# Kernel optimization log

Hardware: AMD Instinct MI355X
Metric: run time of the kernel (lower is better)

Reference implementation:

```python
import jax, jax.numpy as jnp
import numpy as np

D_MODEL = 1024
NUM_HEADS = 16
D_HEAD = D_MODEL // NUM_HEADS
D_FF = 4096
BATCH = 2
SEQ = 2048
EPS = 1e-5


def setup_inputs() -> dict:
    key = jax.random.key(0)
    ks = jax.random.split(key, 10)
    def tn(k, shape, std):
        # truncated normal in [-3*std, 3*std]
        return std * jax.random.truncated_normal(k, -3.0, 3.0, shape, dtype=jnp.float32)
    sd_attn = float(np.sqrt(2.0 / (D_MODEL + D_MODEL)))
    sd_ff1 = float(np.sqrt(2.0 / (D_MODEL + D_FF)))
    sd_ff2 = float(np.sqrt(2.0 / (D_FF + D_MODEL)))
    return {
        "x": jax.random.normal(ks[0], (BATCH, SEQ, D_MODEL), dtype=jnp.float32),
        "Wq": tn(ks[1], (D_MODEL, D_MODEL), sd_attn),
        "Wk": tn(ks[2], (D_MODEL, D_MODEL), sd_attn),
        "Wv": tn(ks[3], (D_MODEL, D_MODEL), sd_attn),
        "Wo": tn(ks[4], (D_MODEL, D_MODEL), sd_attn),
        "W1": tn(ks[5], (D_FF, D_MODEL), sd_ff1),
        "W2": tn(ks[6], (D_MODEL, D_FF), sd_ff2),
        "W3": tn(ks[7], (D_FF, D_MODEL), sd_ff1),
        "g1": tn(ks[8], (D_MODEL,), 1.0),
        "g2": tn(ks[9], (D_MODEL,), 1.0),
    }


def rmsnorm(x, g):
    xf = x.astype(jnp.float32)
    rms = jnp.sqrt(jnp.mean(xf * xf, axis=-1, keepdims=True) + EPS)
    return (xf / rms * g).astype(x.dtype)


def attention(x, Wq, Wk, Wv, Wo):
    B, S, D = x.shape
    def heads(t):  # [B,S,D] -> [B,H,S,dh]
        return t.reshape(B, S, NUM_HEADS, D_HEAD).transpose(0, 2, 1, 3)
    q = heads(jnp.einsum('oi,bsi->bso', Wq, x))
    k = heads(jnp.einsum('oi,bsi->bso', Wk, x))
    v = heads(jnp.einsum('oi,bsi->bso', Wv, x))
    logits = jnp.einsum('bhqd,bhkd->bhqk', q, k)
    mask = jnp.tril(jnp.ones((S, S), dtype=bool))
    logits = jnp.where(mask, logits, -jnp.inf)
    attn = jax.nn.softmax(logits / jnp.sqrt(jnp.float32(D_HEAD)), axis=-1)
    o = jnp.einsum('bhqk,bhkd->bhqd', attn, v)
    o = o.transpose(0, 2, 1, 3).reshape(B, S, D)
    return jnp.einsum('oi,bsi->bso', Wo, o)


def swiglu(x, W1, W2, W3):
    h1 = jnp.einsum('fi,bsi->bsf', W1, x)
    h3 = jnp.einsum('fi,bsi->bsf', W3, x)
    h = h1 * jax.nn.sigmoid(h1) * h3
    return jnp.einsum('of,bsf->bso', W2, h)


def reference(x, Wq, Wk, Wv, Wo, W1, W2, W3, g1, g2):
    x = x + attention(rmsnorm(x, g1), Wq, Wk, Wv, Wo)
    x = x + swiglu(rmsnorm(x, g2), W1, W2, W3)
    return x
```

## Files before the change

kernel.cpp:

```cpp
#include <hip/hip_runtime.h>
#include <hip/hip_bf16.h>

#define DM 1024
#define NH 16
#define DH 64
#define DFF 4096
#define NBATCH 2
#define SEQL 2048
#define MTOK (NBATCH*SEQL)

typedef float f32x4 __attribute__((ext_vector_type(4)));
typedef __bf16 bf16x8 __attribute__((ext_vector_type(8)));
typedef unsigned short u16;
typedef unsigned int u32;
typedef unsigned short u16x4 __attribute__((ext_vector_type(4)));
typedef unsigned short u16x8 __attribute__((ext_vector_type(8)));
typedef unsigned int u32x4 __attribute__((ext_vector_type(4)));

__device__ __forceinline__ u16 f2bf(float f) {
    u32 u = __builtin_bit_cast(u32, f);
    return (u16)((u + 0x7fffu + ((u >> 16) & 1u)) >> 16);
}
__device__ __forceinline__ float bf2f(u16 h) {
    return __builtin_bit_cast(float, (u32)h << 16);
}
__device__ __forceinline__ f32x4 mfma16(bf16x8 a, bf16x8 b, f32x4 c) {
    return __builtin_amdgcn_mfma_f32_16x16x32_bf16(a, b, c, 0, 0, 0);
}
__device__ __forceinline__ void gload16(const void* g, void* l) {
    __builtin_amdgcn_global_load_lds(
        (const __attribute__((address_space(1))) unsigned int*)g,
        (__attribute__((address_space(3))) unsigned int*)l, 16, 0, 0);
}
__device__ __forceinline__ int xcd_swz(int p, int nwg) {
    return (p & 7) * (nwg >> 3) + (p >> 3);
}
#define WAIT_VM8_BAR  { asm volatile("s_waitcnt vmcnt(8)" ::: "memory"); \
                        asm volatile("s_barrier" ::: "memory"); }
#define WAIT_VM0_BAR  { asm volatile("s_waitcnt vmcnt(0)" ::: "memory"); \
                        asm volatile("s_barrier" ::: "memory"); }
#define LGKM0_BAR     { asm volatile("s_waitcnt lgkmcnt(0)" ::: "memory"); \
                        asm volatile("s_barrier" ::: "memory"); }

__device__ __forceinline__ void gemm_core(
    const u16* __restrict__ Ah, const u16* __restrict__ Al,
    const u16* __restrict__ Bh, const u16* __restrict__ Bl,
    int K, int m0, int n0,
    u16* lsAh, u16* lsAl, u16* lsBh, u16* lsBl,
    f32x4 acc[4][4])
{
    const int t = threadIdx.x;
    const int lane = t & 63;
    const int wv = t >> 6;
    const int wm = ((t >> 7) & 1) * 64;
    const int wn = ((t >> 6) & 1) * 64;
    const int lrow = lane & 15;
    const int lk = lane >> 4;
    const f32x4 FZ = {0.f, 0.f, 0.f, 0.f};
#pragma unroll
    for (int i = 0; i < 4; ++i)
#pragma unroll
        for (int j = 0; j < 4; ++j) acc[i][j] = FZ;

    const int NT = K >> 5;
    const int rsub = lane >> 2;
    const int gchk = ((lane & 3) ^ ((lane >> 3) & 3)) * 8;
    const int rsw = (lk ^ ((lrow >> 1) & 3)) * 8;

    auto stage = [&](int buf, int kt) {
        const int k0 = kt << 5;
#pragma unroll
        for (int p = 0; p < 2; ++p) {
            const int seg = wv * 2 + p;
            const int row = seg * 16 + rsub;
            const size_t sa = (size_t)(m0 + row) * K + k0 + gchk;
            const size_t sb = (size_t)(n0 + row) * K + k0 + gchk;
            const int d = buf * 4096 + seg * 512;
            gload16(Ah + sa, lsAh + d);
            gload16(Al + sa, lsAl + d);
            gload16(Bh + sb, lsBh + d);
            gload16(Bl + sb, lsBl + d);
        }
    };

    stage(0, 0);
    int buf = 0;
    for (int kt = 0; kt < NT; ++kt) {
        if (kt + 1 < NT) {
            stage(buf ^ 1, kt + 1);
            WAIT_VM8_BAR
        } else {
            WAIT_VM0_BAR
        }
        bf16x8 ah[4], al[4], bh[4], bl[4];
#pragma unroll
        for (int i = 0; i < 4; ++i) {
            const int ia = buf * 4096 + (wm + i * 16 + lrow) * 32 + rsw;
            ah[i] = *reinterpret_cast<const bf16x8*>(&lsAh[ia]);
            al[i] = *reinterpret_cast<const bf16x8*>(&lsAl[ia]);
            const int ib = buf * 4096 + (wn + i * 16 + lrow) * 32 + rsw;
            bh[i] = *reinterpret_cast<const bf16x8*>(&lsBh[ib]);
            bl[i] = *reinterpret_cast<const bf16x8*>(&lsBl[ib]);
        }
        __builtin_amdgcn_s_setprio(1);
#pragma unroll
        for (int i = 0; i < 4; ++i)
#pragma unroll
            for (int j = 0; j < 4; ++j) {
                acc[i][j] = mfma16(ah[i], bh[j], acc[i][j]);
                acc[i][j] = mfma16(al[i], bh[j], acc[i][j]);
                acc[i][j] = mfma16(ah[i], bl[j], acc[i][j]);
            }
        __builtin_amdgcn_s_setprio(0);
        LGKM0_BAR
        buf ^= 1;
    }
}

#define GEMM_LDS \
    __shared__ __align__(16) u16 lsAh[2 * 4096], lsAl[2 * 4096], \
                                 lsBh[2 * 4096], lsBl[2 * 4096];

template <class F>
__device__ __forceinline__ void epilogue(const f32x4 acc[4][4], int m0, int n0, F f) {
    const int lane = threadIdx.x & 63;
    const int wm = ((threadIdx.x >> 7) & 1) * 64;
    const int wn = ((threadIdx.x >> 6) & 1) * 64;
#pragma unroll
    for (int i = 0; i < 4; ++i)
#pragma unroll
        for (int j = 0; j < 4; ++j)
#pragma unroll
            for (int r = 0; r < 4; ++r) {
                const int m = m0 + wm + i * 16 + ((lane >> 4) << 2) + r;
                const int o = n0 + wn + j * 16 + (lane & 15);
                f(m, o, acc[i][j][r]);
            }
}

struct WJobs { const float* s[7]; u16* h[7]; u16* l[7]; };
__global__ __launch_bounds__(256) void k_splitw_all(WJobs jobs)
{
    const int bid = blockIdx.x;
    int which, off;
    if (bid < 2048) { which = bid >> 9; off = bid & 511; }
    else { which = 4 + ((bid - 2048) >> 11); off = (bid - 2048) & 2047; }
    const float* __restrict__ src = jobs.s[which];
    u16* __restrict__ dh = jobs.h[which];
    u16* __restrict__ dl = jobs.l[which];
    const int i = (off * 256 + threadIdx.x) * 8;
    const f32x4 a = *reinterpret_cast<const f32x4*>(src + i);
    const f32x4 b = *reinterpret_cast<const f32x4*>(src + i + 4);
    u16x8 hh, ll;
#pragma unroll
    for (int e = 0; e < 4; ++e) {
        const u16 h0 = f2bf(a[e]);
        hh[e] = h0; ll[e] = f2bf(a[e] - bf2f(h0));
        const u16 h1 = f2bf(b[e]);
        hh[4 + e] = h1; ll[4 + e] = f2bf(b[e] - bf2f(h1));
    }
    *reinterpret_cast<u16x8*>(dh + i) = hh;
    *reinterpret_cast<u16x8*>(dl + i) = ll;
}

__global__ __launch_bounds__(256) void k_rmsnorm(
    const float* __restrict__ x, const float* __restrict__ g,
    u16* __restrict__ oh, u16* __restrict__ ol)
{
    const int row = blockIdx.x * 4 + (threadIdx.x >> 6);
    const int lane = threadIdx.x & 63;
    const float* xr = x + (size_t)row * DM;
    f32x4 v[4];
    float ss = 0.f;
#pragma unroll
    for (int j = 0; j < 4; ++j) {
        v[j] = *reinterpret_cast<const f32x4*>(&xr[(lane + j * 64) * 4]);
        ss += v[j][0] * v[j][0] + v[j][1] * v[j][1] + v[j][2] * v[j][2] + v[j][3] * v[j][3];
    }
#pragma unroll
    for (int off = 32; off > 0; off >>= 1) ss += __shfl_xor(ss, off, 64);
    const float sc = 1.0f / sqrtf(ss * (1.0f / (float)DM) + 1e-5f);
#pragma unroll
    for (int j = 0; j < 4; ++j) {
        const int c0 = (lane + j * 64) * 4;
        const f32x4 gv = *reinterpret_cast<const f32x4*>(&g[c0]);
        u16x4 hh, ll;
#pragma unroll
        for (int e = 0; e < 4; ++e) {
            const float y = v[j][e] * sc * gv[e];
            const u16 hi = f2bf(y);
            hh[e] = hi;
            ll[e] = f2bf(y - bf2f(hi));
        }
        *reinterpret_cast<u16x4*>(&oh[(size_t)row * DM + c0]) = hh;
        *reinterpret_cast<u16x4*>(&ol[(size_t)row * DM + c0]) = ll;
    }
}

__global__ __launch_bounds__(256, 2) void k_qkv(
    const u16* __restrict__ Ah, const u16* __restrict__ Al,
    const u16* __restrict__ swqh, const u16* __restrict__ swql,
    const u16* __restrict__ swkh, const u16* __restrict__ swkl,
    const u16* __restrict__ swvh, const u16* __restrict__ swvl,
    u16* __restrict__ qh, u16* __restrict__ ql, u16* __restrict__ kh, u16* __restrict__ kl,
    u16* __restrict__ vth, u16* __restrict__ vtl)
{
    GEMM_LDS
    const int swz = xcd_swz(blockIdx.y * 32 + blockIdx.x, 32 * 24);
    const int m0 = (swz & 31) * 128;
    const int ng = (swz >> 5) * 128;
    const int proj = ng >> 10;
    const int n0 = ng & 1023;
    const u16* Bh = (proj == 0) ? swqh : ((proj == 1) ? swkh : swvh);
    const u16* Bl = (proj == 0) ? swql : ((proj == 1) ? swkl : swvl);
    f32x4 acc[4][4];
    gemm_core(Ah, Al, Bh, Bl, DM, m0, n0, lsAh, lsAl, lsBh, lsBl, acc);
    if (proj < 2) {
        u16* oph = (proj == 0) ? qh : kh;
        u16* opl = (proj == 0) ? ql : kl;
        epilogue(acc, m0, n0, [&](int m, int o, float val) {
            const int b = m >> 11, s = m & (SEQL - 1);
            const int hd = o >> 6, d = o & 63;
            const size_t idx = (((size_t)b * NH + hd) * SEQL + s) * DH + d;
            const u16 hi = f2bf(val);
            oph[idx] = hi;
            opl[idx] = f2bf(val - bf2f(hi));
        });
    } else {
        epilogue(acc, m0, n0, [&](int m, int o, float val) {
            const int b = m >> 11, s = m & (SEQL - 1);
            const int hd = o >> 6, d = o & 63;
            const size_t idx = (((size_t)b * NH + hd) * DH + d) * SEQL + s;
            const u16 hi = f2bf(val);
            vth[idx] = hi;
            vtl[idx] = f2bf(val - bf2f(hi));
        });
    }
}

__global__ __launch_bounds__(256, 2) void k_oproj(
    const u16* __restrict__ Ah, const u16* __restrict__ Al,
    const u16* __restrict__ Bh, const u16* __restrict__ Bl,
    const float* __restrict__ xres, float* __restrict__ out)
{
    GEMM_LDS
    const int swz = xcd_swz(blockIdx.y * 32 + blockIdx.x, 32 * 8);
    const int m0 = (swz & 31) * 128;
    const int n0 = (swz >> 5) * 128;
    f32x4 acc[4][4];
    gemm_core(Ah, Al, Bh, Bl, DM, m0, n0, lsAh, lsAl, lsBh, lsBl, acc);
    epilogue(acc, m0, n0, [&](int m, int o, float val) {
        const size_t idx = (size_t)m * DM + o;
        out[idx] = xres[idx] + val;
    });
}

__global__ __launch_bounds__(256, 2) void k_ffn13(
    const u16* __restrict__ Ah, const u16* __restrict__ Al,
    const u16* __restrict__ B1h, const u16* __restrict__ B1l,
    const u16* __restrict__ B3h, const u16* __restrict__ B3l,
    u16* __restrict__ hh, u16* __restrict__ hl)
{
    GEMM_LDS
    const int swz = xcd_swz(blockIdx.y * 32 + blockIdx.x, 32 * 32);
    const int m0 = (swz & 31) * 128;
    const int n0 = (swz >> 5) * 128;
    f32x4 acc1[4][4], acc3[4][4];
    gemm_core(Ah, Al, B1h, B1l, DM, m0, n0, lsAh, lsAl, lsBh, lsBl, acc1);
    gemm_core(Ah, Al, B3h, B3l, DM, m0, n0, lsAh, lsAl, lsBh, lsBl, acc3);
    const int lane = threadIdx.x & 63;
    const int wm = ((threadIdx.x >> 7) & 1) * 64;
    const int wn = ((threadIdx.x >> 6) & 1) * 64;
#pragma unroll
    for (int i = 0; i < 4; ++i)
#pragma unroll
        for (int j = 0; j < 4; ++j)
#pragma unroll
            for (int r = 0; r < 4; ++r) {
                const int m = m0 + wm + i * 16 + ((lane >> 4) << 2) + r;
                const int o = n0 + wn + j * 16 + (lane & 15);
                const float h1 = acc1[i][j][r];
                const float h3 = acc3[i][j][r];
                const float sg = 1.0f / (1.0f + expf(-h1));
                const float hv = h1 * sg * h3;
                const size_t idx = (size_t)m * DFF + o;
                const u16 hi = f2bf(hv);
                hh[idx] = hi;
                hl[idx] = f2bf(hv - bf2f(hi));
            }
}

__global__ __launch_bounds__(256, 2) void k_ffn2(
    const u16* __restrict__ Ah, const u16* __restrict__ Al,
    const u16* __restrict__ Bh, const u16* __restrict__ Bl,
    float* __restrict__ out)
{
    GEMM_LDS
    const int swz = xcd_swz(blockIdx.y * 32 + blockIdx.x, 32 * 8);
    const int m0 = (swz & 31) * 128;
    const int n0 = (swz >> 5) * 128;
    f32x4 acc[4][4];
    gemm_core(Ah, Al, Bh, Bl, DFF, m0, n0, lsAh, lsAl, lsBh, lsBl, acc);
    epilogue(acc, m0, n0, [&](int m, int o, float val) {
        const size_t idx = (size_t)m * DM + o;
        out[idx] = out[idx] + val;
    });
}

__global__ __launch_bounds__(256) void k_attn(
    const u16* __restrict__ gqh, const u16* __restrict__ gql,
    const u16* __restrict__ gkh, const u16* __restrict__ gkl,
    const u16* __restrict__ gvth, const u16* __restrict__ gvtl,
    u16* __restrict__ aoh, u16* __restrict__ aol)
{
    __shared__ __align__(16) u16 sKh[2][4096], sKl[2][4096], sVh[2][4096], sVl[2][4096];
    __shared__ __align__(16) u32 Pw[4][16 * 64];
    const int t = threadIdx.x, lane = t & 63, wid = t >> 6;
    const int lrow = lane & 15, lk = lane >> 4;
    const int swz = xcd_swz(blockIdx.y * 16 + blockIdx.x, 16 * 32);
    const int pr = swz & 15;
    const int bh = swz >> 4;
    const size_t base = (size_t)bh * SEQL * DH;
    const f32x4 FZ = {0.f, 0.f, 0.f, 0.f};
    const int b = bh >> 4, hd = bh & 15;

    auto stage = [&](int buf, int kvt) {
        const int kv0 = kvt << 6;
#pragma unroll
        for (int p = 0; p < 2; ++p) {
            const int seg = wid * 2 + p;
            const int row = seg * 8 + (lane >> 3);
            const int g = (lane & 7) ^ (row & 7);
            const size_t sk = base + (size_t)(kv0 + row) * DH + g * 8;
            const size_t sv = base + (size_t)row * SEQL + kv0 + g * 8;
            gload16(gkh + sk, &sKh[buf][seg * 512]);
            gload16(gkl + sk, &sKl[buf][seg * 512]);
            gload16(gvth + sv, &sVh[buf][seg * 512]);
            gload16(gvtl + sv, &sVl[buf][seg * 512]);
        }
    };

    for (int hf = 0; hf < 2; ++hf) {
        const int qt = hf ? (31 - pr) : pr;
        const int qw = qt * 64 + wid * 16;
        bf16x8 Qh[2], Ql[2];
#pragma unroll
        for (int ks = 0; ks < 2; ++ks) {
            const size_t off = base + (size_t)(qw + lrow) * DH + ks * 32 + lk * 8;
            Qh[ks] = *reinterpret_cast<const bf16x8*>(&gqh[off]);
            Ql[ks] = *reinterpret_cast<const bf16x8*>(&gql[off]);
        }
        float mr[4], lr[4];
        f32x4 Oa[4];
#pragma unroll
        for (int r = 0; r < 4; ++r) { mr[r] = -1.0e30f; lr[r] = 0.f; }
#pragma unroll
        for (int n = 0; n < 4; ++n) Oa[n] = FZ;

        const int ntile = qt + 1;
        stage(0, 0);
        int buf = 0;
        for (int kvt = 0; kvt < ntile; ++kvt) {
            if (kvt + 1 < ntile) {
                stage(buf ^ 1, kvt + 1);
                WAIT_VM8_BAR
            } else {
                WAIT_VM0_BAR
            }
            const int kv0 = kvt << 6;
            f32x4 S[4];
#pragma unroll
            for (int nf = 0; nf < 4; ++nf) S[nf] = FZ;
#pragma unroll
            for (int ks = 0; ks < 2; ++ks) {
                bf16x8 kbh[4], kbl[4];
#pragma unroll
                for (int nf = 0; nf < 4; ++nf) {
                    const int row = nf * 16 + lrow;
                    const int idx = row * 64 + (((lk + ks * 4) ^ (row & 7)) << 3);
                    kbh[nf] = *reinterpret_cast<const bf16x8*>(&sKh[buf][idx]);
                    kbl[nf] = *reinterpret_cast<const bf16x8*>(&sKl[buf][idx]);
                }
                __builtin_amdgcn_s_setprio(1);
#pragma unroll
                for (int nf = 0; nf < 4; ++nf) {
                    S[nf] = mfma16(Qh[ks], kbh[nf], S[nf]);
                    S[nf] = mfma16(Ql[ks], kbh[nf], S[nf]);
                    S[nf] = mfma16(Qh[ks], kbl[nf], S[nf]);
                }
                __builtin_amdgcn_s_setprio(0);
            }
#pragma unroll
            for (int r = 0; r < 4; ++r) {
                const int qrow = qw + (lk << 2) + r;
                float rmx = -3.0e38f;
#pragma unroll
                for (int nf = 0; nf < 4; ++nf) {
                    const int col = kv0 + nf * 16 + lrow;
                    const float tv = (col <= qrow) ? S[nf][r] * 0.125f : -3.0e38f;
                    S[nf][r] = tv;
                    rmx = fmaxf(rmx, tv);
                }
#pragma unroll
                for (int off = 8; off > 0; off >>= 1) rmx = fmaxf(rmx, __shfl_xor(rmx, off, 16));
                const float mnew = fmaxf(mr[r], rmx);
                const float alpha = exp2f((mr[r] - mnew) * 1.44269504f);
                mr[r] = mnew;
                float rsum = 0.f;
#pragma unroll
                for (int nf = 0; nf < 4; ++nf) {
                    const float p = exp2f((S[nf][r] - mnew) * 1.44269504f);
                    S[nf][r] = p;
                    rsum += p;
                }
#pragma unroll
                for (int off = 8; off > 0; off >>= 1) rsum += __shfl_xor(rsum, off, 16);
                lr[r] = lr[r] * alpha + rsum;
#pragma unroll
                for (int n = 0; n < 4; ++n) Oa[n][r] *= alpha;
                const int prow = (lk << 2) + r;
#pragma unroll
                for (int nf = 0; nf < 4; ++nf) {
                    const float p = S[nf][r];
                    const u16 phi = f2bf(p);
                    const u16 plo = f2bf(p - bf2f(phi));
                    const int pcol = nf * 16 + lrow;
                    Pw[wid][prow * 64 + ((((pcol >> 3) ^ (prow & 7))) << 3) + (pcol & 7)] =
                        (u32)phi | ((u32)plo << 16);
                }
            }
            asm volatile("s_waitcnt lgkmcnt(0)" ::: "memory");
#pragma unroll
            for (int ks = 0; ks < 2; ++ks) {
                const int row = lrow;
                const int c = (lk + ks * 4) ^ (row & 7);
                const u32* pp = &Pw[wid][row * 64 + (c << 3)];
                const u32x4 w0 = *reinterpret_cast<const u32x4*>(pp);
                const u32x4 w1 = *reinterpret_cast<const u32x4*>(pp + 4);
                union { u16 s[8]; bf16x8 v; } uh, ul;
#pragma unroll
                for (int e = 0; e < 4; ++e) {
                    uh.s[e] = (u16)(w0[e] & 0xffffu); ul.s[e] = (u16)(w0[e] >> 16);
                    uh.s[e + 4] = (u16)(w1[e] & 0xffffu); ul.s[e + 4] = (u16)(w1[e] >> 16);
                }
                bf16x8 vbh[4], vbl[4];
#pragma unroll
                for (int n = 0; n < 4; ++n) {
                    const int vr = n * 16 + lrow;
                    const int idx = vr * 64 + (((lk + ks * 4) ^ (vr & 7)) << 3);
                    vbh[n] = *reinterpret_cast<const bf16x8*>(&sVh[buf][idx]);
                    vbl[n] = *reinterpret_cast<const bf16x8*>(&sVl[buf][idx]);
                }
                __builtin_amdgcn_s_setprio(1);
#pragma unroll
                for (int n = 0; n < 4; ++n) {
                    Oa[n] = mfma16(uh.v, vbh[n], Oa[n]);
                    Oa[n] = mfma16(ul.v, vbh[n], Oa[n]);
                    Oa[n] = mfma16(uh.v, vbl[n], Oa[n]);
                }
                __builtin_amdgcn_s_setprio(0);
            }
            LGKM0_BAR
            buf ^= 1;
        }
#pragma unroll
        for (int r = 0; r < 4; ++r) {
            const float inv = 1.0f / lr[r];
            const int s = qw + (lk << 2) + r;
#pragma unroll
            for (int n = 0; n < 4; ++n) {
                const float o = Oa[n][r] * inv;
                const int d = hd * 64 + n * 16 + lrow;
                const size_t idx = ((size_t)b * SEQL + s) * DM + d;
                const u16 hi = f2bf(o);
                aoh[idx] = hi;
                aol[idx] = f2bf(o - bf2f(hi));
            }
        }
    }
}

extern "C" void kernel_launch(void* const* d_in, const int* in_sizes, int n_in,
                              void* d_out, int out_size, void* d_ws, size_t ws_size,
                              hipStream_t stream) {
    (void)in_sizes; (void)n_in; (void)out_size; (void)ws_size;
    const float* x  = (const float*)d_in[0];
    const float* Wq = (const float*)d_in[1];
    const float* Wk = (const float*)d_in[2];
    const float* Wv = (const float*)d_in[3];
    const float* Wo = (const float*)d_in[4];
    const float* W1 = (const float*)d_in[5];
    const float* W2 = (const float*)d_in[6];
    const float* W3 = (const float*)d_in[7];
    const float* g1 = (const float*)d_in[8];
    const float* g2 = (const float*)d_in[9];
    float* out = (float*)d_out;
    char* w = (char*)d_ws;
    const size_t MB = 1024ull * 1024ull;
    u16* xnh = (u16*)(w + 0 * MB);
    u16* xnl = (u16*)(w + 8 * MB);
    u16* qh  = (u16*)(w + 16 * MB);
    u16* ql  = (u16*)(w + 24 * MB);
    u16* kh  = (u16*)(w + 32 * MB);
    u16* kl  = (u16*)(w + 40 * MB);
    u16* vth = (u16*)(w + 48 * MB);
    u16* vtl = (u16*)(w + 56 * MB);
    u16* aoh = (u16*)(w + 64 * MB);
    u16* aol = (u16*)(w + 72 * MB);
    u16* hh  = (u16*)(w + 16 * MB);
    u16* hl  = (u16*)(w + 48 * MB);
    u16* wsp = (u16*)(w + 80 * MB);
    u16* wqh = wsp;                  u16* wql = wqh + (1u << 20);
    u16* wkh = wql + (1u << 20);     u16* wkl = wkh + (1u << 20);
    u16* wvh = wkl + (1u << 20);     u16* wvl = wvh + (1u << 20);
    u16* woh = wvl + (1u << 20);     u16* wol = woh + (1u << 20);
    u16* w1h = wol + (1u << 20);     u16* w1l = w1h + (4u << 20);
    u16* w2h = w1l + (4u << 20);     u16* w2l = w2h + (4u << 20);
    u16* w3h = w2l + (4u << 20);     u16* w3l = w3h + (4u << 20);

    WJobs jobs;
    jobs.s[0] = Wq; jobs.h[0] = wqh; jobs.l[0] = wql;
    jobs.s[1] = Wk; jobs.h[1] = wkh; jobs.l[1] = wkl;
    jobs.s[2] = Wv; jobs.h[2] = wvh; jobs.l[2] = wvl;
    jobs.s[3] = Wo; jobs.h[3] = woh; jobs.l[3] = wol;
    jobs.s[4] = W1; jobs.h[4] = w1h; jobs.l[4] = w1l;
    jobs.s[5] = W2; jobs.h[5] = w2h; jobs.l[5] = w2l;
    jobs.s[6] = W3; jobs.h[6] = w3h; jobs.l[6] = w3l;
    k_splitw_all<<<8192, 256, 0, stream>>>(jobs);

    k_rmsnorm<<<dim3(MTOK / 4), 256, 0, stream>>>(x, g1, xnh, xnl);
    k_qkv<<<dim3(32, 24), 256, 0, stream>>>(xnh, xnl,
        wqh, wql, wkh, wkl, wvh, wvl, qh, ql, kh, kl, vth, vtl);
    k_attn<<<dim3(16, 32), 256, 0, stream>>>(qh, ql, kh, kl, vth, vtl, aoh, aol);
    k_oproj<<<dim3(32, 8), 256, 0, stream>>>(aoh, aol, woh, wol, x, out);
    k_rmsnorm<<<dim3(MTOK / 4), 256, 0, stream>>>(out, g2, xnh, xnl);
    k_ffn13<<<dim3(32, 32), 256, 0, stream>>>(xnh, xnl, w1h, w1l, w3h, w3l, hh, hl);
    k_ffn2<<<dim3(32, 8), 256, 0, stream>>>(hh, hl, w2h, w2l, out);
}
```

Baseline: 762.8 us.

## Use 256x128 tiles with 8 waves for QKV and FFN13 GEMMs

Adds a 512-thread GEMM core whose block computes a 256x128 output tile, so the B tile staged in LDS is shared by twice as many rows. QKV and FFN1/3 switch to it, with fewer blocks and one block per CU. The XCD-aware block swizzle is also removed from all GEMMs in favour of plain blockIdx mapping. The cost is lower occupancy and worse L2 locality across XCDs.

```diff
diff --git a/kernel.cpp b/kernel.cpp
--- a/kernel.cpp
+++ b/kernel.cpp
@@ -36,6 +36,8 @@
     return (p & 7) * (nwg >> 3) + (p >> 3);
 }
 #define WAIT_VM8_BAR  { asm volatile("s_waitcnt vmcnt(8)" ::: "memory"); \
+                        asm volatile("s_barrier" ::: "memory"); }
+#define WAIT_VM6_BAR  { asm volatile("s_waitcnt vmcnt(6)" ::: "memory"); \
                         asm volatile("s_barrier" ::: "memory"); }
 #define WAIT_VM0_BAR  { asm volatile("s_waitcnt vmcnt(0)" ::: "memory"); \
                         asm volatile("s_barrier" ::: "memory"); }
@@ -121,11 +123,96 @@
     __shared__ __align__(16) u16 lsAh[2 * 4096], lsAl[2 * 4096], \
                                  lsBh[2 * 4096], lsBl[2 * 4096];
 
-template <class F>
+__device__ __forceinline__ void gemm_core256(
+    const u16* __restrict__ Ah, const u16* __restrict__ Al,
+    const u16* __restrict__ Bh, const u16* __restrict__ Bl,
+    int K, int m0, int n0,
+    u16* lsAh, u16* lsAl,
+    u16* lsBh, u16* lsBl,
+    f32x4 acc[4][4])
+{
+    const int t = threadIdx.x;
+    const int lane = t & 63;
+    const int wv = t >> 6;
+    const int wm = (wv >> 1) * 64;
+    const int wn = (wv & 1) * 64;
+    const int lrow = lane & 15;
+    const int lk = lane >> 4;
+    const f32x4 FZ = {0.f, 0.f, 0.f, 0.f};
+#pragma unroll
+    for (int i = 0; i < 4; ++i)
+#pragma unroll
+        for (int j = 0; j < 4; ++j) acc[i][j] = FZ;
+
+    const int NT = K >> 5;
+    const int rsub = lane >> 2;
+    const int gchk = ((lane & 3) ^ ((lane >> 3) & 3)) * 8;
+    const int rsw = (lk ^ ((lrow >> 1) & 3)) * 8;
+
+    auto stage = [&](int buf, int kt) {
+        const int k0 = kt << 5;
+#pragma unroll
+        for (int p = 0; p < 2; ++p) {
+            const int seg = wv + p * 8;
+            const int row = seg * 16 + rsub;
+            const size_t sa = (size_t)(m0 + row) * K + k0 + gchk;
+            const int d = buf * 8192 + seg * 512;
+            gload16(Ah + sa, lsAh + d);
+            gload16(Al + sa, lsAl + d);
+        }
+        {
+            const int row = wv * 16 + rsub;
+            const size_t sb = (size_t)(n0 + row) * K + k0 + gchk;
+            const int d = buf * 4096 + wv * 512;
+            gload16(Bh + sb, lsBh + d);
+            gload16(Bl + sb, lsBl + d);
+        }
+    };
+
+    stage(0, 0);
+    int buf = 0;
+    for (int kt = 0; kt < NT; ++kt) {
+        if (kt + 1 < NT) {
+            stage(buf ^ 1, kt + 1);
+            WAIT_VM6_BAR
+        } else {
+            WAIT_VM0_BAR
+        }
+        bf16x8 ah[4], al[4], bh[4], bl[4];
+#pragma unroll
+        for (int i = 0; i < 4; ++i) {
+            const int ia = buf * 8192 + (wm + i * 16 + lrow) * 32 + rsw;
+            ah[i] = *reinterpret_cast<const bf16x8*>(&lsAh[ia]);
+            al[i] = *reinterpret_cast<const bf16x8*>(&lsAl[ia]);
+            const int ib = buf * 4096 + (wn + i * 16 + lrow) * 32 + rsw;
+            bh[i] = *reinterpret_cast<const bf16x8*>(&lsBh[ib]);
+            bl[i] = *reinterpret_cast<const bf16x8*>(&lsBl[ib]);
+        }
+        __builtin_amdgcn_s_setprio(1);
+#pragma unroll
+        for (int i = 0; i < 4; ++i)
+#pragma unroll
+            for (int j = 0; j < 4; ++j) {
+                acc[i][j] = mfma16(ah[i], bh[j], acc[i][j]);
+                acc[i][j] = mfma16(al[i], bh[j], acc[i][j]);
+                acc[i][j] = mfma16(ah[i], bl[j], acc[i][j]);
+            }
+        __builtin_amdgcn_s_setprio(0);
+        LGKM0_BAR
+        buf ^= 1;
+    }
+}
+
+#define GEMM_LDS256 \
+    __shared__ __align__(16) u16 lsAh[2 * 8192], lsAl[2 * 8192], \
+                                 lsBh[2 * 4096], lsBl[2 * 4096];
+
+template <int WAVES, class F>
 __device__ __forceinline__ void epilogue(const f32x4 acc[4][4], int m0, int n0, F f) {
     const int lane = threadIdx.x & 63;
-    const int wm = ((threadIdx.x >> 7) & 1) * 64;
-    const int wn = ((threadIdx.x >> 6) & 1) * 64;
+    const int wv = (int)threadIdx.x >> 6;
+    const int wm = (WAVES == 8 ? (wv >> 1) : ((wv >> 1) & 1)) * 64;
+    const int wn = (wv & 1) * 64;
 #pragma unroll
     for (int i = 0; i < 4; ++i)
 #pragma unroll
@@ -197,7 +284,7 @@
     }
 }
 
-__global__ __launch_bounds__(256, 2) void k_qkv(
+__global__ __launch_bounds__(512, 1) void k_qkv(
     const u16* __restrict__ Ah, const u16* __restrict__ Al,
     const u16* __restrict__ swqh, const u16* __restrict__ swql,
     const u16* __restrict__ swkh, const u16* __restrict__ swkl,
@@ -205,20 +292,19 @@
     u16* __restrict__ qh, u16* __restrict__ ql, u16* __restrict__ kh, u16* __restrict__ kl,
     u16* __restrict__ vth, u16* __restrict__ vtl)
 {
-    GEMM_LDS
-    const int swz = xcd_swz(blockIdx.y * 32 + blockIdx.x, 32 * 24);
-    const int m0 = (swz & 31) * 128;
-    const int ng = (swz >> 5) * 128;
+    GEMM_LDS256
+    const int m0 = blockIdx.x * 256;
+    const int ng = blockIdx.y * 128;
     const int proj = ng >> 10;
     const int n0 = ng & 1023;
     const u16* Bh = (proj == 0) ? swqh : ((proj == 1) ? swkh : swvh);
     const u16* Bl = (proj == 0) ? swql : ((proj == 1) ? swkl : swvl);
     f32x4 acc[4][4];
-    gemm_core(Ah, Al, Bh, Bl, DM, m0, n0, lsAh, lsAl, lsBh, lsBl, acc);
+    gemm_core256(Ah, Al, Bh, Bl, DM, m0, n0, lsAh, lsAl, lsBh, lsBl, acc);
     if (proj < 2) {
         u16* oph = (proj == 0) ? qh : kh;
         u16* opl = (proj == 0) ? ql : kl;
-        epilogue(acc, m0, n0, [&](int m, int o, float val) {
+        epilogue<8>(acc, m0, n0, [&](int m, int o, float val) {
             const int b = m >> 11, s = m & (SEQL - 1);
             const int hd = o >> 6, d = o & 63;
             const size_t idx = (((size_t)b * NH + hd) * SEQL + s) * DH + d;
@@ -227,7 +313,7 @@
             opl[idx] = f2bf(val - bf2f(hi));
         });
     } else {
-        epilogue(acc, m0, n0, [&](int m, int o, float val) {
+        epilogue<8>(acc, m0, n0, [&](int m, int o, float val) {
             const int b = m >> 11, s = m & (SEQL - 1);
             const int hd = o >> 6, d = o & 63;
             const size_t idx = (((size_t)b * NH + hd) * DH + d) * SEQL + s;
@@ -244,33 +330,32 @@
     const float* __restrict__ xres, float* __restrict__ out)
 {
     GEMM_LDS
-    const int swz = xcd_swz(blockIdx.y * 32 + blockIdx.x, 32 * 8);
-    const int m0 = (swz & 31) * 128;
-    const int n0 = (swz >> 5) * 128;
+    const int m0 = blockIdx.x * 128;
+    const int n0 = blockIdx.y * 128;
     f32x4 acc[4][4];
     gemm_core(Ah, Al, Bh, Bl, DM, m0, n0, lsAh, lsAl, lsBh, lsBl, acc);
-    epilogue(acc, m0, n0, [&](int m, int o, float val) {
+    epilogue<4>(acc, m0, n0, [&](int m, int o, float val) {
         const size_t idx = (size_t)m * DM + o;
         out[idx] = xres[idx] + val;
     });
 }
 
-__global__ __launch_bounds__(256, 2) void k_ffn13(
+__global__ __launch_bounds__(512, 1) void k_ffn13(
     const u16* __restrict__ Ah, const u16* __restrict__ Al,
     const u16* __restrict__ B1h, const u16* __restrict__ B1l,
     const u16* __restrict__ B3h, const u16* __restrict__ B3l,
     u16* __restrict__ hh, u16* __restrict__ hl)
 {
-    GEMM_LDS
-    const int swz = xcd_swz(blockIdx.y * 32 + blockIdx.x, 32 * 32);
-    const int m0 = (swz & 31) * 128;
-    const int n0 = (swz >> 5) * 128;
+    GEMM_LDS256
+    const int m0 = blockIdx.x * 256;
+    const int n0 = blockIdx.y * 128;
     f32x4 acc1[4][4], acc3[4][4];
-    gemm_core(Ah, Al, B1h, B1l, DM, m0, n0, lsAh, lsAl, lsBh, lsBl, acc1);
-    gemm_core(Ah, Al, B3h, B3l, DM, m0, n0, lsAh, lsAl, lsBh, lsBl, acc3);
+    gemm_core256(Ah, Al, B1h, B1l, DM, m0, n0, lsAh, lsAl, lsBh, lsBl, acc1);
+    gemm_core256(Ah, Al, B3h, B3l, DM, m0, n0, lsAh, lsAl, lsBh, lsBl, acc3);
     const int lane = threadIdx.x & 63;
-    const int wm = ((threadIdx.x >> 7) & 1) * 64;
-    const int wn = ((threadIdx.x >> 6) & 1) * 64;
+    const int wv = (int)threadIdx.x >> 6;
+    const int wm = (wv >> 1) * 64;
+    const int wn = (wv & 1) * 64;
 #pragma unroll
     for (int i = 0; i < 4; ++i)
 #pragma unroll
@@ -296,12 +381,11 @@
     float* __restrict__ out)
 {
     GEMM_LDS
-    const int swz = xcd_swz(blockIdx.y * 32 + blockIdx.x, 32 * 8);
-    const int m0 = (swz & 31) * 128;
-    const int n0 = (swz >> 5) * 128;
+    const int m0 = blockIdx.x * 128;
+    const int n0 = blockIdx.y * 128;
     f32x4 acc[4][4];
     gemm_core(Ah, Al, Bh, Bl, DFF, m0, n0, lsAh, lsAl, lsBh, lsBl, acc);
-    epilogue(acc, m0, n0, [&](int m, int o, float val) {
+    epilogue<4>(acc, m0, n0, [&](int m, int o, float val) {
         const size_t idx = (size_t)m * DM + o;
         out[idx] = out[idx] + val;
     });
@@ -529,11 +613,11 @@
     k_splitw_all<<<8192, 256, 0, stream>>>(jobs);
 
     k_rmsnorm<<<dim3(MTOK / 4), 256, 0, stream>>>(x, g1, xnh, xnl);
-    k_qkv<<<dim3(32, 24), 256, 0, stream>>>(xnh, xnl,
+    k_qkv<<<dim3(16, 24), 512, 0, stream>>>(xnh, xnl,
         wqh, wql, wkh, wkl, wvh, wvl, qh, ql, kh, kl, vth, vtl);
     k_attn<<<dim3(16, 32), 256, 0, stream>>>(qh, ql, kh, kl, vth, vtl, aoh, aol);
     k_oproj<<<dim3(32, 8), 256, 0, stream>>>(aoh, aol, woh, wol, x, out);
     k_rmsnorm<<<dim3(MTOK / 4), 256, 0, stream>>>(out, g2, xnh, xnl);
-    k_ffn13<<<dim3(32, 32), 256, 0, stream>>>(xnh, xnl, w1h, w1l, w3h, w3l, hh, hl);
+    k_ffn13<<<dim3(16, 32), 512, 0, stream>>>(xnh, xnl, w1h, w1l, w3h, w3l, hh, hl);
     k_ffn2<<<dim3(32, 8), 256, 0, stream>>>(hh, hl, w2h, w2l, out);
 }
```

Result: no change. 759.7 us (-0.4%).
